# Kernel tuning notes

Measured on AMD Instinct MI355X. Metric: run time of the kernel, lower is better.

## Reference

```python
import jax, jax.numpy as jnp
import numpy as np

B, T, C = 2, 4096, 512
H = 8
MEMORY = 256  # window: key j visible to query i iff 0 <= i - j <= MEMORY


def setup_inputs() -> dict:
    key = jax.random.key(0)
    k1, k2, k3 = jax.random.split(key, 3)
    x = jax.random.normal(k1, (B, T, C), dtype=jnp.float32)
    w_attn = jax.random.normal(k2, (3 * C, C), dtype=jnp.float32) * 0.02
    w_proj = jax.random.normal(k3, (C, C), dtype=jnp.float32) * 0.02
    return {"x": x, "w_attn": w_attn, "w_proj": w_proj}


def reference(x, w_attn, w_proj):
    b, t, c = x.shape
    d = c // H
    # fused QKV projection (Linear without bias): x @ W^T
    qkv = jnp.einsum('btc,fc->btf', x, w_attn)  # [B,T,3C]
    q, k, v = jnp.split(qkv, 3, axis=-1)
    # [B,T,C] -> [B,H,T,d]
    q = q.reshape(b, t, H, d).transpose(0, 2, 1, 3)
    k = k.reshape(b, t, H, d).transpose(0, 2, 1, 3)
    v = v.reshape(b, t, H, d).transpose(0, 2, 1, 3)
    # sliding-window causal mask: tril(0) & ~tril(-memory-1)
    i = jnp.arange(t)[:, None]
    j = jnp.arange(t)[None, :]
    mask = (j <= i) & (i - j <= MEMORY)  # [T,T] bool
    scores = jnp.einsum('bhqd,bhkd->bhqk', q, k) * (1.0 / np.sqrt(d))
    scores = jnp.where(mask, scores, -jnp.inf)
    attn = jax.nn.softmax(scores, axis=-1)
    y = jnp.einsum('bhqk,bhkd->bhqd', attn, v)  # [B,H,T,d]
    y = y.transpose(0, 2, 1, 3).reshape(b, t, c)
    # output projection
    y = jnp.einsum('btc,fc->btf', y, w_proj)
    return y
```

## Files before the change

kernel.cpp:

```cpp
#include <hip/hip_runtime.h>
#include <hip/hip_bf16.h>
#include <stdint.h>

#define BB 2
#define TT 4096
#define CC 512
#define HH 8
#define DD 64
#define MEM 256

typedef unsigned short u16;
typedef __bf16 bf16x8 __attribute__((ext_vector_type(8)));
typedef float floatx4 __attribute__((ext_vector_type(4)));

__device__ inline u16 f2bf(float f) {
  uint32_t u = __float_as_uint(f);
  uint32_t r = (u + 0x7fffu + ((u >> 16) & 1u)) >> 16;
  return (u16)r;
}

__device__ inline void gld16(const u16* g, u16* lds) {
  __builtin_amdgcn_global_load_lds(
      (const __attribute__((address_space(1))) uint32_t*)g,
      (__attribute__((address_space(3))) uint32_t*)lds, 16, 0, 0);
}

__global__ __launch_bounds__(256) void cvt_f32_bf16(const float* __restrict__ s,
                                                    u16* __restrict__ d, int n) {
  int i = (blockIdx.x * 256 + threadIdx.x) * 4;
  if (i >= n) return;
  float4 v = *reinterpret_cast<const float4*>(s + i);
  ushort4 o;
  o.x = f2bf(v.x); o.y = f2bf(v.y); o.z = f2bf(v.z); o.w = f2bf(v.w);
  *reinterpret_cast<ushort4*>(d + i) = o;
}

template <bool OUT_F32>
__global__ __launch_bounds__(256) void gemm_bt(const u16* __restrict__ A,
                                               const u16* __restrict__ Bw,
                                               void* __restrict__ Cout,
                                               int M, int N, int K) {
  __shared__ __align__(16) u16 As[128 * 32];
  __shared__ __align__(16) u16 Bs[128 * 32];
  const int tid = threadIdx.x;
  const int w = tid >> 6, lane = tid & 63, quad = lane >> 4, l16 = lane & 15;
  const int wm = w >> 1, wn = w & 1;
  const int m0 = blockIdx.x * 128, n0 = blockIdx.y * 128;

  floatx4 acc[4][4] = {};
  const int nK = K >> 5;
  for (int kb = 0; kb < nK; ++kb) {
    const int kof = kb * 32;
    {
      int c = tid;
      gld16(A + (size_t)(m0 + (c >> 2)) * K + kof + (c & 3) * 8, As + (size_t)c * 8);
      c = tid + 256;
      gld16(A + (size_t)(m0 + (c >> 2)) * K + kof + (c & 3) * 8, As + (size_t)c * 8);
      c = tid;
      gld16(Bw + (size_t)(n0 + (c >> 2)) * K + kof + (c & 3) * 8, Bs + (size_t)c * 8);
      c = tid + 256;
      gld16(Bw + (size_t)(n0 + (c >> 2)) * K + kof + (c & 3) * 8, Bs + (size_t)c * 8);
    }
    __syncthreads();
    bf16x8 af[4], bfr[4];
#pragma unroll
    for (int i = 0; i < 4; i++)
      af[i] = *reinterpret_cast<const bf16x8*>(&As[(wm * 64 + i * 16 + l16) * 32 + quad * 8]);
#pragma unroll
    for (int i = 0; i < 4; i++)
      bfr[i] = *reinterpret_cast<const bf16x8*>(&Bs[(wn * 64 + i * 16 + l16) * 32 + quad * 8]);
#pragma unroll
    for (int mi = 0; mi < 4; mi++)
#pragma unroll
      for (int ni = 0; ni < 4; ni++)
        acc[mi][ni] = __builtin_amdgcn_mfma_f32_16x16x32_bf16(af[mi], bfr[ni], acc[mi][ni], 0, 0, 0);
    __syncthreads();
  }
#pragma unroll
  for (int mi = 0; mi < 4; mi++) {
    int row = m0 + wm * 64 + mi * 16 + quad * 4;
#pragma unroll
    for (int ni = 0; ni < 4; ni++) {
      int col = n0 + wn * 64 + ni * 16 + l16;
#pragma unroll
      for (int r = 0; r < 4; r++) {
        if (OUT_F32)
          ((float*)Cout)[(size_t)(row + r) * N + col] = acc[mi][ni][r];
        else
          ((u16*)Cout)[(size_t)(row + r) * N + col] = f2bf(acc[mi][ni][r]);
      }
    }
  }
}

__global__ __launch_bounds__(256) void attn_win(const u16* __restrict__ qkv,
                                                u16* __restrict__ y) {
  const int q0 = blockIdx.x * 64;
  const int h = blockIdx.y;
  const int b = blockIdx.z;
  const int tid = threadIdx.x;
  const int w = tid >> 6, lane = tid & 63, quad = lane >> 4, l16 = lane & 15;

  __shared__ __align__(16) u16 Qs[64 * 64];
  __shared__ __align__(16) u16 Ks[64 * 64];
  __shared__ __align__(16) u16 Vt[64 * 72];
  __shared__ __align__(16) u16 Ps[4][16 * 72];

  const size_t baseQ = ((size_t)(b * TT + q0)) * 1536 + h * 64;
  {
    int c = tid;
    gld16(qkv + baseQ + (size_t)(c >> 3) * 1536 + (c & 7) * 8, Qs + (size_t)c * 8);
    c = tid + 256;
    gld16(qkv + baseQ + (size_t)(c >> 3) * 1536 + (c & 7) * 8, Qs + (size_t)c * 8);
  }
  __syncthreads();
  bf16x8 qf0 = *reinterpret_cast<const bf16x8*>(&Qs[(w * 16 + l16) * 64 + quad * 8]);
  bf16x8 qf1 = *reinterpret_cast<const bf16x8*>(&Qs[(w * 16 + l16) * 64 + 32 + quad * 8]);

  floatx4 acc_o[4] = {};
  float m_run[4], l_run[4];
#pragma unroll
  for (int r = 0; r < 4; r++) { m_run[r] = -1e30f; l_run[r] = 0.f; }

  const int s_min = (q0 >= 256) ? 0 : ((256 - q0) >> 6);
  for (int s = s_min; s < 5; ++s) {
    const int k0 = q0 - 256 + s * 64;
    const size_t baseK = ((size_t)(b * TT + k0)) * 1536 + 512 + h * 64;
    {
      int c = tid;
      gld16(qkv + baseK + (size_t)(c >> 3) * 1536 + (c & 7) * 8, Ks + (size_t)c * 8);
      c = tid + 256;
      gld16(qkv + baseK + (size_t)(c >> 3) * 1536 + (c & 7) * 8, Ks + (size_t)c * 8);
    }
    const size_t baseV = ((size_t)(b * TT + k0)) * 1536 + 1024 + h * 64;
#pragma unroll
    for (int half = 0; half < 2; ++half) {
      int c = tid + half * 256;
      int key = c >> 3, dc = c & 7;
      const u16* src = qkv + baseV + (size_t)key * 1536 + dc * 8;
      u16 tmp[8];
      *reinterpret_cast<uint4*>(tmp) = *reinterpret_cast<const uint4*>(src);
#pragma unroll
      for (int e = 0; e < 8; e++) Vt[(dc * 8 + e) * 72 + key] = tmp[e];
    }
    __syncthreads();

    floatx4 sc[4] = {};
#pragma unroll
    for (int nt = 0; nt < 4; nt++) {
      bf16x8 b0 = *reinterpret_cast<const bf16x8*>(&Ks[(nt * 16 + l16) * 64 + quad * 8]);
      bf16x8 b1 = *reinterpret_cast<const bf16x8*>(&Ks[(nt * 16 + l16) * 64 + 32 + quad * 8]);
      sc[nt] = __builtin_amdgcn_mfma_f32_16x16x32_bf16(qf0, b0, sc[nt], 0, 0, 0);
      sc[nt] = __builtin_amdgcn_mfma_f32_16x16x32_bf16(qf1, b1, sc[nt], 0, 0, 0);
    }
#pragma unroll
    for (int nt = 0; nt < 4; nt++) {
#pragma unroll
      for (int r = 0; r < 4; r++) {
        int i = q0 + w * 16 + quad * 4 + r;
        int j = k0 + nt * 16 + l16;
        float v = sc[nt][r] * 0.125f;
        bool vis = (j <= i) && (i - j <= MEM);
        sc[nt][r] = vis ? v : -1e30f;
      }
    }
    float mt[4];
#pragma unroll
    for (int r = 0; r < 4; r++) {
      float m = fmaxf(fmaxf(sc[0][r], sc[1][r]), fmaxf(sc[2][r], sc[3][r]));
      m = fmaxf(m, __shfl_xor(m, 1));
      m = fmaxf(m, __shfl_xor(m, 2));
      m = fmaxf(m, __shfl_xor(m, 4));
      m = fmaxf(m, __shfl_xor(m, 8));
      mt[r] = m;
    }
#pragma unroll
    for (int r = 0; r < 4; r++) {
      float mn = fmaxf(m_run[r], mt[r]);
      float alpha = __expf(m_run[r] - mn);
      float lsum = 0.f;
#pragma unroll
      for (int nt = 0; nt < 4; nt++) {
        float p = __expf(sc[nt][r] - mn);
        sc[nt][r] = p;
        lsum += p;
      }
      lsum += __shfl_xor(lsum, 1);
      lsum += __shfl_xor(lsum, 2);
      lsum += __shfl_xor(lsum, 4);
      lsum += __shfl_xor(lsum, 8);
      l_run[r] = l_run[r] * alpha + lsum;
      m_run[r] = mn;
#pragma unroll
      for (int nt = 0; nt < 4; nt++) acc_o[nt][r] *= alpha;
    }
#pragma unroll
    for (int nt = 0; nt < 4; nt++)
#pragma unroll
      for (int r = 0; r < 4; r++)
        Ps[w][(quad * 4 + r) * 72 + nt * 16 + l16] = f2bf(sc[nt][r]);
#pragma unroll
    for (int ki = 0; ki < 2; ki++) {
      bf16x8 pf = *reinterpret_cast<const bf16x8*>(&Ps[w][l16 * 72 + ki * 32 + quad * 8]);
#pragma unroll
      for (int nt = 0; nt < 4; nt++) {
        bf16x8 vf = *reinterpret_cast<const bf16x8*>(&Vt[(nt * 16 + l16) * 72 + ki * 32 + quad * 8]);
        acc_o[nt] = __builtin_amdgcn_mfma_f32_16x16x32_bf16(pf, vf, acc_o[nt], 0, 0, 0);
      }
    }
    __syncthreads();
  }
#pragma unroll
  for (int r = 0; r < 4; r++) {
    float inv = 1.f / l_run[r];
    int row = q0 + w * 16 + quad * 4 + r;
    size_t base = (size_t)(b * TT + row) * 512 + h * 64;
#pragma unroll
    for (int nt = 0; nt < 4; nt++)
      y[base + nt * 16 + l16] = f2bf(acc_o[nt][r] * inv);
  }
}

extern "C" void kernel_launch(void* const* d_in, const int* in_sizes, int n_in,
                              void* d_out, int out_size, void* d_ws, size_t ws_size,
                              hipStream_t stream) {
  const float* x = (const float*)d_in[0];
  const float* w_attn = (const float*)d_in[1];
  const float* w_proj = (const float*)d_in[2];
  float* out = (float*)d_out;

  u16* xb = (u16*)d_ws;
  u16* wab = xb + (size_t)8192 * 512;
  u16* wpb = wab + (size_t)1536 * 512;
  u16* qkv = wpb + (size_t)512 * 512;
  u16* yb = qkv + (size_t)8192 * 1536;

  const int nx = 8192 * 512;
  const int nwa = 1536 * 512;
  const int nwp = 512 * 512;
  cvt_f32_bf16<<<nx / 1024, 256, 0, stream>>>(x, xb, nx);
  cvt_f32_bf16<<<nwa / 1024, 256, 0, stream>>>(w_attn, wab, nwa);
  cvt_f32_bf16<<<nwp / 1024, 256, 0, stream>>>(w_proj, wpb, nwp);

  gemm_bt<false><<<dim3(64, 12), 256, 0, stream>>>(xb, wab, (void*)qkv, 8192, 1536, 512);
  attn_win<<<dim3(TT / 64, HH, BB), 256, 0, stream>>>(qkv, yb);
  gemm_bt<true><<<dim3(64, 4), 256, 0, stream>>>(yb, wpb, (void*)out, 8192, 512, 512);
}
```

Measured before the change: 147.8 us.

## Fuse conversions, swizzle attention LDS, trim masking, use smaller-N output GEMM

Replaces the three f32-to-bf16 conversion launches with one combined kernel. The attention kernel now XOR-swizzles Q, K and V tiles in LDS to avoid bank conflicts and folds the 1/sqrt(d) scale into Q in bf16. It also applies the mask only on the first and last key blocks. The output projection uses a new 128x64-tile GEMM to double block count for better CU occupancy. Scaling Q in bf16 adds a small rounding change relative to scaling the fp32 scores.

```diff
diff --git a/kernel.cpp b/kernel.cpp
--- a/kernel.cpp
+++ b/kernel.cpp
@@ -6,7 +6,6 @@
 #define TT 4096
 #define CC 512
 #define HH 8
-#define DD 64
 #define MEM 256
 
 typedef unsigned short u16;
@@ -25,14 +24,21 @@
       (__attribute__((address_space(3))) uint32_t*)lds, 16, 0, 0);
 }
 
-__global__ __launch_bounds__(256) void cvt_f32_bf16(const float* __restrict__ s,
-                                                    u16* __restrict__ d, int n) {
-  int i = (blockIdx.x * 256 + threadIdx.x) * 4;
-  if (i >= n) return;
-  float4 v = *reinterpret_cast<const float4*>(s + i);
+__global__ __launch_bounds__(256) void cvt_all(const float* __restrict__ x,
+                                               const float* __restrict__ wa,
+                                               const float* __restrict__ wp,
+                                               u16* __restrict__ xb,
+                                               u16* __restrict__ wab,
+                                               u16* __restrict__ wpb) {
+  int i = blockIdx.x * 256 + threadIdx.x;
+  const float* s; u16* d; int off;
+  if (i < 1048576) { s = x; d = xb; off = i; }
+  else if (i < 1245184) { s = wa; d = wab; off = i - 1048576; }
+  else { s = wp; d = wpb; off = i - 1245184; }
+  float4 v = *reinterpret_cast<const float4*>(s + (size_t)off * 4);
   ushort4 o;
   o.x = f2bf(v.x); o.y = f2bf(v.y); o.z = f2bf(v.z); o.w = f2bf(v.w);
-  *reinterpret_cast<ushort4*>(d + i) = o;
+  *reinterpret_cast<ushort4*>(d + (size_t)off * 4) = o;
 }
 
 template <bool OUT_F32>
@@ -93,6 +99,56 @@
   }
 }
 
+__global__ __launch_bounds__(256) void gemm_bt_n64(const u16* __restrict__ A,
+                                                   const u16* __restrict__ Bw,
+                                                   float* __restrict__ C,
+                                                   int M, int N, int K) {
+  __shared__ __align__(16) u16 As[128 * 32];
+  __shared__ __align__(16) u16 Bs[64 * 32];
+  const int tid = threadIdx.x;
+  const int w = tid >> 6, lane = tid & 63, quad = lane >> 4, l16 = lane & 15;
+  const int m0 = blockIdx.x * 128, n0 = blockIdx.y * 64;
+
+  floatx4 acc[2][4] = {};
+  const int nK = K >> 5;
+  for (int kb = 0; kb < nK; ++kb) {
+    const int kof = kb * 32;
+    {
+      int c = tid;
+      gld16(A + (size_t)(m0 + (c >> 2)) * K + kof + (c & 3) * 8, As + (size_t)c * 8);
+      c = tid + 256;
+      gld16(A + (size_t)(m0 + (c >> 2)) * K + kof + (c & 3) * 8, As + (size_t)c * 8);
+      c = tid;
+      gld16(Bw + (size_t)(n0 + (c >> 2)) * K + kof + (c & 3) * 8, Bs + (size_t)c * 8);
+    }
+    __syncthreads();
+    bf16x8 af[2], bfr[4];
+#pragma unroll
+    for (int i = 0; i < 2; i++)
+      af[i] = *reinterpret_cast<const bf16x8*>(&As[(w * 32 + i * 16 + l16) * 32 + quad * 8]);
+#pragma unroll
+    for (int i = 0; i < 4; i++)
+      bfr[i] = *reinterpret_cast<const bf16x8*>(&Bs[(i * 16 + l16) * 32 + quad * 8]);
+#pragma unroll
+    for (int mi = 0; mi < 2; mi++)
+#pragma unroll
+      for (int ni = 0; ni < 4; ni++)
+        acc[mi][ni] = __builtin_amdgcn_mfma_f32_16x16x32_bf16(af[mi], bfr[ni], acc[mi][ni], 0, 0, 0);
+    __syncthreads();
+  }
+#pragma unroll
+  for (int mi = 0; mi < 2; mi++) {
+    int row = m0 + w * 32 + mi * 16 + quad * 4;
+#pragma unroll
+    for (int ni = 0; ni < 4; ni++) {
+      int col = n0 + ni * 16 + l16;
+#pragma unroll
+      for (int r = 0; r < 4; r++)
+        C[(size_t)(row + r) * N + col] = acc[mi][ni][r];
+    }
+  }
+}
+
 __global__ __launch_bounds__(256) void attn_win(const u16* __restrict__ qkv,
                                                 u16* __restrict__ y) {
   const int q0 = blockIdx.x * 64;
@@ -108,14 +164,20 @@
 
   const size_t baseQ = ((size_t)(b * TT + q0)) * 1536 + h * 64;
   {
-    int c = tid;
-    gld16(qkv + baseQ + (size_t)(c >> 3) * 1536 + (c & 7) * 8, Qs + (size_t)c * 8);
-    c = tid + 256;
-    gld16(qkv + baseQ + (size_t)(c >> 3) * 1536 + (c & 7) * 8, Qs + (size_t)c * 8);
+    int c = tid, row = c >> 3, blk = (c & 7) ^ (row & 7);
+    gld16(qkv + baseQ + (size_t)row * 1536 + blk * 8, Qs + (size_t)c * 8);
+    c = tid + 256; row = c >> 3; blk = (c & 7) ^ (row & 7);
+    gld16(qkv + baseQ + (size_t)row * 1536 + blk * 8, Qs + (size_t)c * 8);
   }
   __syncthreads();
-  bf16x8 qf0 = *reinterpret_cast<const bf16x8*>(&Qs[(w * 16 + l16) * 64 + quad * 8]);
-  bf16x8 qf1 = *reinterpret_cast<const bf16x8*>(&Qs[(w * 16 + l16) * 64 + 32 + quad * 8]);
+  const int qrow = w * 16 + l16;
+  bf16x8 qf0 = *reinterpret_cast<const bf16x8*>(&Qs[qrow * 64 + (quad ^ (l16 & 7)) * 8]);
+  bf16x8 qf1 = *reinterpret_cast<const bf16x8*>(&Qs[qrow * 64 + ((quad + 4) ^ (l16 & 7)) * 8]);
+#pragma unroll
+  for (int e = 0; e < 8; e++) {
+    qf0[e] = qf0[e] * (__bf16)0.125f;
+    qf1[e] = qf1[e] * (__bf16)0.125f;
+  }
 
   floatx4 acc_o[4] = {};
   float m_run[4], l_run[4];
@@ -127,44 +189,47 @@
     const int k0 = q0 - 256 + s * 64;
     const size_t baseK = ((size_t)(b * TT + k0)) * 1536 + 512 + h * 64;
     {
-      int c = tid;
-      gld16(qkv + baseK + (size_t)(c >> 3) * 1536 + (c & 7) * 8, Ks + (size_t)c * 8);
-      c = tid + 256;
-      gld16(qkv + baseK + (size_t)(c >> 3) * 1536 + (c & 7) * 8, Ks + (size_t)c * 8);
+      int c = tid, row = c >> 3, blk = (c & 7) ^ (row & 7);
+      gld16(qkv + baseK + (size_t)row * 1536 + blk * 8, Ks + (size_t)c * 8);
+      c = tid + 256; row = c >> 3; blk = (c & 7) ^ (row & 7);
+      gld16(qkv + baseK + (size_t)row * 1536 + blk * 8, Ks + (size_t)c * 8);
     }
     const size_t baseV = ((size_t)(b * TT + k0)) * 1536 + 1024 + h * 64;
 #pragma unroll
     for (int half = 0; half < 2; ++half) {
       int c = tid + half * 256;
       int key = c >> 3, dc = c & 7;
-      const u16* src = qkv + baseV + (size_t)key * 1536 + dc * 8;
       u16 tmp[8];
-      *reinterpret_cast<uint4*>(tmp) = *reinterpret_cast<const uint4*>(src);
-#pragma unroll
-      for (int e = 0; e < 8; e++) Vt[(dc * 8 + e) * 72 + key] = tmp[e];
+      *reinterpret_cast<uint4*>(tmp) =
+          *reinterpret_cast<const uint4*>(qkv + baseV + (size_t)key * 1536 + dc * 8);
+      int col = key ^ (dc * 8);
+#pragma unroll
+      for (int e = 0; e < 8; e++) Vt[(dc * 8 + e) * 72 + col] = tmp[e];
     }
     __syncthreads();
 
     floatx4 sc[4] = {};
 #pragma unroll
     for (int nt = 0; nt < 4; nt++) {
-      bf16x8 b0 = *reinterpret_cast<const bf16x8*>(&Ks[(nt * 16 + l16) * 64 + quad * 8]);
-      bf16x8 b1 = *reinterpret_cast<const bf16x8*>(&Ks[(nt * 16 + l16) * 64 + 32 + quad * 8]);
+      int krow = nt * 16 + l16;
+      bf16x8 b0 = *reinterpret_cast<const bf16x8*>(&Ks[krow * 64 + (quad ^ (l16 & 7)) * 8]);
+      bf16x8 b1 = *reinterpret_cast<const bf16x8*>(&Ks[krow * 64 + ((quad + 4) ^ (l16 & 7)) * 8]);
       sc[nt] = __builtin_amdgcn_mfma_f32_16x16x32_bf16(qf0, b0, sc[nt], 0, 0, 0);
       sc[nt] = __builtin_amdgcn_mfma_f32_16x16x32_bf16(qf1, b1, sc[nt], 0, 0, 0);
     }
-#pragma unroll
-    for (int nt = 0; nt < 4; nt++) {
-#pragma unroll
-      for (int r = 0; r < 4; r++) {
-        int i = q0 + w * 16 + quad * 4 + r;
-        int j = k0 + nt * 16 + l16;
-        float v = sc[nt][r] * 0.125f;
-        bool vis = (j <= i) && (i - j <= MEM);
-        sc[nt][r] = vis ? v : -1e30f;
-      }
-    }
-    float mt[4];
+    if (s == 4) {
+#pragma unroll
+      for (int nt = 0; nt < 4; nt++)
+#pragma unroll
+        for (int r = 0; r < 4; r++)
+          if (w * 16 + quad * 4 + r < nt * 16 + l16) sc[nt][r] = -1e30f;
+    } else if (s == 0) {
+#pragma unroll
+      for (int nt = 0; nt < 4; nt++)
+#pragma unroll
+        for (int r = 0; r < 4; r++)
+          if (w * 16 + quad * 4 + r > nt * 16 + l16) sc[nt][r] = -1e30f;
+    }
 #pragma unroll
     for (int r = 0; r < 4; r++) {
       float m = fmaxf(fmaxf(sc[0][r], sc[1][r]), fmaxf(sc[2][r], sc[3][r]));
@@ -172,11 +237,7 @@
       m = fmaxf(m, __shfl_xor(m, 2));
       m = fmaxf(m, __shfl_xor(m, 4));
       m = fmaxf(m, __shfl_xor(m, 8));
-      mt[r] = m;
-    }
-#pragma unroll
-    for (int r = 0; r < 4; r++) {
-      float mn = fmaxf(m_run[r], mt[r]);
+      float mn = fmaxf(m_run[r], m);
       float alpha = __expf(m_run[r] - mn);
       float lsum = 0.f;
 #pragma unroll
@@ -204,7 +265,9 @@
       bf16x8 pf = *reinterpret_cast<const bf16x8*>(&Ps[w][l16 * 72 + ki * 32 + quad * 8]);
 #pragma unroll
       for (int nt = 0; nt < 4; nt++) {
-        bf16x8 vf = *reinterpret_cast<const bf16x8*>(&Vt[(nt * 16 + l16) * 72 + ki * 32 + quad * 8]);
+        int d = nt * 16 + l16;
+        bf16x8 vf = *reinterpret_cast<const bf16x8*>(
+            &Vt[d * 72 + ((ki * 32 + quad * 8) ^ (d & 56))]);
         acc_o[nt] = __builtin_amdgcn_mfma_f32_16x16x32_bf16(pf, vf, acc_o[nt], 0, 0, 0);
       }
     }
@@ -235,14 +298,8 @@
   u16* qkv = wpb + (size_t)512 * 512;
   u16* yb = qkv + (size_t)8192 * 1536;
 
-  const int nx = 8192 * 512;
-  const int nwa = 1536 * 512;
-  const int nwp = 512 * 512;
-  cvt_f32_bf16<<<nx / 1024, 256, 0, stream>>>(x, xb, nx);
-  cvt_f32_bf16<<<nwa / 1024, 256, 0, stream>>>(w_attn, wab, nwa);
-  cvt_f32_bf16<<<nwp / 1024, 256, 0, stream>>>(w_proj, wpb, nwp);
-
+  cvt_all<<<5120, 256, 0, stream>>>(x, w_attn, w_proj, xb, wab, wpb);
   gemm_bt<false><<<dim3(64, 12), 256, 0, stream>>>(xb, wab, (void*)qkv, 8192, 1536, 512);
   attn_win<<<dim3(TT / 64, HH, BB), 256, 0, stream>>>(qkv, yb);
-  gemm_bt<true><<<dim3(64, 4), 256, 0, stream>>>(yb, wpb, (void*)out, 8192, 512, 512);
-}
+  gemm_bt_n64<<<dim3(64, 8), 256, 0, stream>>>(yb, wpb, out, 8192, 512, 512);
+}
```

Measured after the change: 134.4 us. 1.1x faster.
